# Kernel tuning notes

Hardware: AMD Instinct MI355X
Metric: run time of the kernel (lower is better)

The kernel has to match this reference:

```python
import jax, jax.numpy as jnp
import numpy as np

# model constants (from source: PRE/COMM/OUT sizes; chosen: G, D, E, T, NF)
G, D, E, T = 128, 64, 8, 4096          # group feats, per-elevator feats, n elevators, timesteps
PRE, CI, CH, OUT, NF = 256, 128, 128, 128, 64
ROUNDS, DROPOFF = 3, 0.333
IN = G + D                              # elevator_input_size = 192
OIN = 2 * CH + IN                       # out-LSTM input = 448


def _cell(x, h, c, Wih, Whh, b):
    # torch nn.LSTM cell, gate order i,f,g,o; b = b_ih + b_hh
    g = x @ Wih.T + h @ Whh.T + b
    i, f, gg, o = jnp.split(g, 4, axis=-1)
    c2 = jax.nn.sigmoid(f) * c + jax.nn.sigmoid(i) * jnp.tanh(gg)
    h2 = jax.nn.sigmoid(o) * jnp.tanh(c2)
    return h2, c2


def _forward(features, pre_h0, pre_c0, out_h0, out_c0,
             Wih_p0, Whh_p0, b_p0, Wih_p1, Whh_p1, b_p1, Wfc, bfc,
             Wih_c0, Whh_c0, b_c0, Wih_c1, Whh_c1, b_c1,
             Wih_o, Whh_o, b_o, Wtar, btar, Wdir, bdir):
    def step(carry, feat):
        pre_h, pre_c, out_h, out_c = carry
        group = feat[:G]
        ele = feat[G:].reshape(E, D)
        x = jnp.concatenate([jnp.broadcast_to(group, (E, G)), ele], axis=-1)  # [E, IN]
        # preprocess: 2-layer LSTM single step, batched over elevators
        h0, c0 = _cell(x, pre_h[:, 0], pre_c[:, 0], Wih_p0, Whh_p0, b_p0)
        h1, c1 = _cell(h0, pre_h[:, 1], pre_c[:, 1], Wih_p1, Whh_p1, b_p1)
        pre_out = jax.nn.leaky_relu(h1 @ Wfc.T + bfc, 0.05)                   # [E, CI]
        new_pre_h = jnp.stack([h0, h1], axis=1)
        new_pre_c = jnp.stack([c0, c1], axis=1)
        # alpha-decayed communication rounds: sequential scan over elevators
        ch = jnp.zeros((2, CH), jnp.float32)
        cc = jnp.zeros((2, CH), jnp.float32)
        alpha = 1.0
        for _ in range(ROUNDS):
            def comm_step(cs, xin, alpha=alpha):
                ch_, cc_ = cs
                h0n, c0n = _cell(xin, ch_[0], cc_[0], Wih_c0, Whh_c0, b_c0)
                h0b = (1.0 - alpha) * ch_[0] + alpha * h0n
                c0b = (1.0 - alpha) * cc_[0] + alpha * c0n
                h1n, c1n = _cell(h0b, ch_[1], cc_[1], Wih_c1, Whh_c1, b_c1)
                h1b = (1.0 - alpha) * ch_[1] + alpha * h1n
                c1b = (1.0 - alpha) * cc_[1] + alpha * c1n
                return (jnp.stack([h0b, h1b]), jnp.stack([c0b, c1b])), None
            (ch, cc), _ = jax.lax.scan(comm_step, (ch, cc), pre_out)
            alpha *= DROPOFF
        group_dec = cc.reshape(-1)                                            # [2*CH] = comm_c.flatten()
        out_in = jnp.concatenate([jnp.broadcast_to(group_dec, (E, 2 * CH)), x], axis=-1)  # [E, OIN]
        oh, oc = _cell(out_in, out_h, out_c, Wih_o, Whh_o, b_o)
        tar = jax.nn.softmax(oh @ Wtar.T + btar, axis=-1)                     # [E, NF]
        dr = jax.nn.softmax(oh @ Wdir.T + bdir, axis=-1)                      # [E, 3]
        return (new_pre_h, new_pre_c, oh, oc), (tar, dr)

    _, (tar_seq, dir_seq) = jax.lax.scan(step, (pre_h0, pre_c0, out_h0, out_c0), features)
    return tar_seq, dir_seq


def setup_inputs() -> dict:
    key = jax.random.key(0)
    ks = iter(jax.random.split(key, 32))
    p = lambda *s: jax.random.normal(next(ks), s, jnp.float32) * 0.05
    return {
        "features": jax.random.normal(next(ks), (T, G + E * D), jnp.float32),
        "pre_h0": jnp.zeros((E, 2, PRE), jnp.float32),
        "pre_c0": jnp.zeros((E, 2, PRE), jnp.float32),
        "out_h0": jnp.zeros((E, OUT), jnp.float32),
        "out_c0": jnp.zeros((E, OUT), jnp.float32),
        "Wih_p0": p(4 * PRE, IN), "Whh_p0": p(4 * PRE, PRE), "b_p0": p(4 * PRE),
        "Wih_p1": p(4 * PRE, PRE), "Whh_p1": p(4 * PRE, PRE), "b_p1": p(4 * PRE),
        "Wfc": p(CI, PRE), "bfc": p(CI),
        "Wih_c0": p(4 * CH, CI), "Whh_c0": p(4 * CH, CH), "b_c0": p(4 * CH),
        "Wih_c1": p(4 * CH, CH), "Whh_c1": p(4 * CH, CH), "b_c1": p(4 * CH),
        "Wih_o": p(4 * OUT, OIN), "Whh_o": p(4 * OUT, OUT), "b_o": p(4 * OUT),
        "Wtar": p(NF, OUT), "btar": p(NF),
        "Wdir": p(3, OUT), "bdir": p(3),
    }


def reference(features, pre_h0, pre_c0, out_h0, out_c0,
              Wih_p0, Whh_p0, b_p0, Wih_p1, Whh_p1, b_p1, Wfc, bfc,
              Wih_c0, Whh_c0, b_c0, Wih_c1, Whh_c1, b_c1,
              Wih_o, Whh_o, b_o, Wtar, btar, Wdir, bdir):
    return _forward(features, pre_h0, pre_c0, out_h0, out_c0,
                    Wih_p0, Whh_p0, b_p0, Wih_p1, Whh_p1, b_p1, Wfc, bfc,
                    Wih_c0, Whh_c0, b_c0, Wih_c1, Whh_c1, b_c1,
                    Wih_o, Whh_o, b_o, Wtar, btar, Wdir, bdir)
```

## Files before the change

### kernel.cpp

```cpp
#include <hip/hip_runtime.h>
#include <hip/hip_bf16.h>

#define T_   4096
#define E_   8
#define NCON 176

typedef unsigned long long ull;

__device__ __forceinline__ float sigm(float x)  { return 1.0f / (1.0f + __expf(-x)); }
__device__ __forceinline__ float tanh_(float x) { return 1.0f - 2.0f / (__expf(2.0f * x) + 1.0f); }

__device__ __forceinline__ ull aload64(const ull* p) {
  return __hip_atomic_load(p, __ATOMIC_RELAXED, __HIP_MEMORY_SCOPE_AGENT);
}
__device__ __forceinline__ int aload32(const int* p) {
  return __hip_atomic_load(p, __ATOMIC_RELAXED, __HIP_MEMORY_SCOPE_AGENT);
}
__device__ __forceinline__ float aloadf(const float* p) {
  return __hip_atomic_load(p, __ATOMIC_RELAXED, __HIP_MEMORY_SCOPE_AGENT);
}
__device__ __forceinline__ void lbar() {
  asm volatile("s_waitcnt lgkmcnt(0)\n\ts_barrier" ::: "memory");
}

#define FMA_8(ACC, W, VA, VB)                                   \
  ACC[0] = fmaf((W), (VA).x, ACC[0]); ACC[1] = fmaf((W), (VA).y, ACC[1]); \
  ACC[2] = fmaf((W), (VA).z, ACC[2]); ACC[3] = fmaf((W), (VA).w, ACC[3]); \
  ACC[4] = fmaf((W), (VB).x, ACC[4]); ACC[5] = fmaf((W), (VB).y, ACC[5]); \
  ACC[6] = fmaf((W), (VB).z, ACC[6]); ACC[7] = fmaf((W), (VB).w, ACC[7]);

__global__ void initK(const float* __restrict__ Wih_p0, const float* __restrict__ Whh_p0,
                      const float* __restrict__ Wih_p1, const float* __restrict__ Whh_p1,
                      const float* __restrict__ Wih_c0, const float* __restrict__ Whh_c0,
                      const float* __restrict__ Wih_c1, const float* __restrict__ Whh_c1,
                      const float* __restrict__ Wih_o,
                      float* wt_p0, float* wt_p1, float* wt_c0, float* wt_c1,
                      float* wt_o1, float* wt_o2, int* flags) {
  const int NW = 458752 + 524288 + 131072 + 131072 + 131072 + 98304;
  const int NF = 2 * 64 * 32 * 32 + 512 * 32;
  const int NTOT = NW + NF;
  const int gsz = gridDim.x * blockDim.x;
  for (int i = blockIdx.x * blockDim.x + threadIdx.x; i < NTOT; i += gsz) {
    int idx = i;
    if (idx < 458752) { int k = idx >> 10, c = idx & 1023;
      int wg = c >> 5, r5 = c & 31, gate = r5 >> 3, jl = r5 & 7;
      int col = gate * 256 + wg * 8 + jl;
      wt_p0[idx] = (k < 192) ? Wih_p0[col * 192 + k] : Whh_p0[col * 256 + (k - 192)]; continue; }
    idx -= 458752;
    if (idx < 524288) { int k = idx >> 10, c = idx & 1023;
      int wg = c >> 5, r5 = c & 31, gate = r5 >> 3, jl = r5 & 7;
      int col = gate * 256 + wg * 8 + jl;
      wt_p1[idx] = (k < 256) ? Wih_p1[col * 256 + k] : Whh_p1[col * 256 + (k - 256)]; continue; }
    idx -= 524288;
    if (idx < 131072) { int k = idx >> 9, r = idx & 511;
      wt_c0[idx] = (k < 128) ? Wih_c0[r * 128 + k] : Whh_c0[r * 128 + (k - 128)]; continue; }
    idx -= 131072;
    if (idx < 131072) { int k = idx >> 9, r = idx & 511;
      wt_c1[idx] = (k < 128) ? Wih_c1[r * 128 + k] : Whh_c1[r * 128 + (k - 128)]; continue; }
    idx -= 131072;
    if (idx < 131072) { int k = idx >> 9, r = idx & 511;
      wt_o1[idx] = Wih_o[r * 448 + k]; continue; }
    idx -= 131072;
    if (idx < 98304) { int k = idx >> 9, r = idx & 511;
      wt_o2[idx] = Wih_o[r * 448 + 256 + k]; continue; }
    idx -= 98304;
    flags[idx] = 0;
  }
}

__global__ void opre2K(const float* __restrict__ feat, const float* __restrict__ wt_o2,
                       __hip_bfloat16* __restrict__ opre2) {
  __shared__ float xb[192 * 8];
  const int t = blockIdx.x, tid = threadIdx.x;
  const float* ft = feat + (size_t)t * 640;
  for (int idx = tid; idx < 192 * 8; idx += 256) {
    int k = idx >> 3, e = idx & 7;
    xb[idx] = (k < 128) ? ft[k] : ft[128 + e * 64 + (k - 128)];
  }
  __syncthreads();
  const int r = tid;
  float A0[8] = {0,0,0,0,0,0,0,0};
  float A1[8] = {0,0,0,0,0,0,0,0};
  const float4* x4 = (const float4*)xb;
  #pragma unroll 2
  for (int k = 0; k < 192; ++k) {
    float w0 = wt_o2[k * 512 + r];
    float w1 = wt_o2[k * 512 + 256 + r];
    float4 a = x4[k * 2], b = x4[k * 2 + 1];
    FMA_8(A0, w0, a, b);
    FMA_8(A1, w1, a, b);
  }
  #pragma unroll
  for (int e = 0; e < 8; ++e) {
    opre2[((size_t)t * 8 + e) * 512 + r]       = __float2bfloat16(A0[e]);
    opre2[((size_t)t * 8 + e) * 512 + 256 + r] = __float2bfloat16(A1[e]);
  }
}

__device__ __forceinline__ void comm_cell(
// ... 21 lines not shown
    FMA_8(A0, w0, a, b);
    FMA_8(A1, w1, a, b);
  }
  {
    float4* g4 = (float4*)glb;
    g4[r * 2]             = make_float4(A0[0], A0[1], A0[2], A0[3]);
    g4[r * 2 + 1]         = make_float4(A0[4], A0[5], A0[6], A0[7]);
    g4[(256 + r) * 2]     = make_float4(A1[0], A1[1], A1[2], A1[3]);
    g4[(256 + r) * 2 + 1] = make_float4(A1[4], A1[5], A1[6], A1[7]);
  }
  __syncthreads();
  for (int idx = tid; idx < 1024; idx += 256) {
    int jj = idx >> 3, tt = idx & 7;
    float gi = glb[jj * 8 + tt]         + bias[jj];
    float gf = glb[(128 + jj) * 8 + tt] + bias[128 + jj];
    float gg = glb[(256 + jj) * 8 + tt] + bias[256 + jj];
    float go = glb[(384 + jj) * 8 + tt] + bias[384 + jj];
    float cold = cL[idx], hold = hL[idx];
    float c2 = sigm(gf) * cold + sigm(gi) * tanh_(gg);
    float h2 = sigm(go) * tanh_(c2);
    float hb = fmaf(alpha, h2 - hold, hold);
    float cb = fmaf(alpha, c2 - cold, cold);
    hL[idx] = hb; cL[idx] = cb;
    if (hout) hout[idx] = hb;
  }
  __syncthreads();
}

__launch_bounds__(256, 1)
__global__ void megaK(const float* __restrict__ feat,
                      const float* __restrict__ pre_h0, const float* __restrict__ pre_c0,
                      const float* __restrict__ wt_p0, const float* __restrict__ wt_p1,
                      const float* __restrict__ b_p0, const float* __restrict__ b_p1,
                      float* __restrict__ h0ring, float* __restrict__ h1ring,
                      float* __restrict__ h1all,
                      int* __restrict__ flagsA, int* __restrict__ flagsB,
                      const float* __restrict__ Wfc, const float* __restrict__ bfc,
                      const float* __restrict__ wt_c0, const float* __restrict__ wt_c1,
                      const float* __restrict__ b_c0, const float* __restrict__ b_c1,
                      const float* __restrict__ wt_o1, const float* __restrict__ b_o,
                      float* __restrict__ opre1, int* __restrict__ flagC,
                      const __hip_bfloat16* __restrict__ opre2,
                      const float* __restrict__ Whh_o, const float* __restrict__ out_h0,
                      const float* __restrict__ out_c0, float* __restrict__ oh_g) {
  __shared__ float lds[38912];
  const int wg = blockIdx.x, tid = threadIdx.x;

  if (wg < 32) {
    float* wl   = lds;
    float* xbuf = lds + 14336;
    float* hsf  = lds + 15872;
    float* gl   = lds + 17920;
    const int r5 = tid & 31, kq = tid >> 5;
    for (int idx = tid; idx < 14336; idx += 256)
      wl[idx] = wt_p0[(size_t)(idx >> 5) * 1024 + wg * 32 + (idx & 31)];
    float creg = 0.f, bi = 0.f, bff = 0.f, bg = 0.f, bo = 0.f;
    if (tid < 64) {
      const int jl = tid >> 3, e = tid & 7, j = wg * 8 + jl;
      creg = pre_c0[(e * 2 + 0) * 256 + j];
      bi = b_p0[j]; bff = b_p0[256 + j]; bg = b_p0[512 + j]; bo = b_p0[768 + j];
    }
    for (int idx = tid; idx < 2048; idx += 256) {
      int k = idx >> 3, e = idx & 7;
      hsf[idx] = pre_h0[(e * 2 + 0) * 256 + k];
    }
    for (int idx = tid; idx < 1536; idx += 256) {
      int k = idx >> 3, e = idx & 7;
      xbuf[idx] = (k < 128) ? feat[k] : feat[128 + e * 64 + (k - 128)];
    }
    __syncthreads();
    float Ax[8] = {0,0,0,0,0,0,0,0};
    {
      const float4* x4 = (const float4*)xbuf;
      #pragma unroll
      for (int k = kq * 24; k < kq * 24 + 24; ++k) {
        float w = wl[k * 32 + r5];
        float4 a = x4[k * 2], b = x4[k * 2 + 1];
        FMA_8(Ax, w, a, b);
      }
    }
    for (int t = 0; t < T_; ++t) {
      float px[6];
      if (t + 1 < T_) {
        const float* ft1 = feat + (size_t)(t + 1) * 640;
        #pragma unroll
        for (int i = 0; i < 6; ++i) {
          int idx = tid + i * 256; int k = idx >> 3, e = idx & 7;
          px[i] = (k < 128) ? ft1[k] : ft1[128 + e * 64 + (k - 128)];
        }
      }
      float A[8];
      #pragma unroll
      for (int i = 0; i < 8; ++i) A[i] = Ax[i];
      {
        const float4* h4 = (const float4*)hsf;
        #pragma unroll
        for (int k2 = 0; k2 < 32; ++k2) {
          const int k = kq * 32 + k2;
          float w = wl[(192 + k) * 32 + r5];
          float4 a = h4[k * 2], b = h4[k * 2 + 1];
          FMA_8(A, w, a, b);
        }
      }
      {
        float4* g4 = (float4*)gl;
        g4[(kq * 32 + r5) * 2]     = make_float4(A[0], A[1], A[2], A[3]);
        g4[(kq * 32 + r5) * 2 + 1] = make_float4(A[4], A[5], A[6], A[7]);
      }
      if (tid >= 224 && t >= 8) {
        const int* fp = flagsB + ((size_t)((t - 8) & 63) * 32 + (tid - 224)) * 32;
        while (aload32(fp) < t - 7) __builtin_amdgcn_s_sleep(1);
      }
      lbar();
      if (tid < 64) {
        float s0 = 0.f, s1 = 0.f, s2 = 0.f, s3 = 0.f;
        #pragma unroll
        for (int q = 0; q < 8; ++q) {
          s0 += gl[q * 256 + tid];       s1 += gl[q * 256 + 64 + tid];
          s2 += gl[q * 256 + 128 + tid]; s3 += gl[q * 256 + 192 + tid];
        }
        float c2 = sigm(s1 + bff) * creg + sigm(s0 + bi) * tanh_(s2 + bg);
        float h2 = sigm(s3 + bo) * tanh_(c2);
        creg = c2;
        __hip_atomic_store(&h0ring[(size_t)(t & 7) * 2048 + wg * 64 + tid], h2,
                           __ATOMIC_RELAXED, __HIP_MEMORY_SCOPE_AGENT);
        asm volatile("s_waitcnt vmcnt(0)" ::: "memory");
        if (tid == 0)
          __hip_atomic_store(&flagsA[((size_t)(t & 63) * 32 + wg) * 32], t + 1,
                             __ATOMIC_RELAXED, __HIP_MEMORY_SCOPE_AGENT);
      }
      if (t + 1 >= T_) break;
      #pragma unroll
      for (int i = 0; i < 6; ++i) xbuf[tid + i * 256] = px[i];
      if (tid >= 64 && tid < 96) {
        const int* fp = flagsA + ((size_t)(t & 63) * 32 + (tid - 64)) * 32;
        while (aload32(fp) < t + 1) __builtin_amdgcn_s_sleep(1);
      }
      lbar();
      ull v[4];
      {
        const ull* s8 = (const ull*)(h0ring + (size_t)(t & 7) * 2048);
        #pragma unroll
        for (int i = 0; i < 4; ++i) v[i] = aload64(s8 + tid * 4 + i);
      }
      #pragma unroll
      for (int i = 0; i < 8; ++i) Ax[i] = 0.f;
      {
        const float4* x4 = (const float4*)xbuf;
        #pragma unroll
        for (int k = kq * 24; k < kq * 24 + 24; ++k) {
          float w = wl[k * 32 + r5];
          float4 a = x4[k * 2], b = x4[k * 2 + 1];
          FMA_8(Ax, w, a, b);
        }
      }
      {
        ull* d8 = (ull*)hsf;
        #pragma unroll
        for (int i = 0; i < 4; ++i) d8[tid * 4 + i] = v[i];
      }
      lbar();
    }
  } else if (wg < 64) {
    const int wgl = wg - 32;
    float* wl  = lds;
    float* xh0 = lds + 16384;
    float* hsf = lds + 18432;
    float* gl  = lds + 20480;
    const int r5 = tid & 31, kq = tid >> 5;
    for (int idx = tid; idx < 16384; idx += 256)
      wl[idx] = wt_p1[(size_t)(idx >> 5) * 1024 + wgl * 32 + (idx & 31)];
    float creg = 0.f, bi = 0.f, bff = 0.f, bg = 0.f, bo = 0.f;
    if (tid < 64) {
      const int jl = tid >> 3, e = tid & 7, j = wgl * 8 + jl;
      creg = pre_c0[(e * 2 + 1) * 256 + j];
      bi = b_p1[j]; bff = b_p1[256 + j]; bg = b_p1[512 + j]; bo = b_p1[768 + j];
    }
    for (int idx = tid; idx < 2048; idx += 256) {
      int k = idx >> 3, e = idx & 7;
      hsf[idx] = pre_h0[(e * 2 + 1) * 256 + k];
    }
    __syncthreads();
    if (tid >= 64 && tid < 128) {
      const int lane = tid - 64;
      const int slot = lane >> 5, b = lane & 31;
      const int* fp = flagsA + ((size_t)slot * 32 + b) * 32;
      while (aload32(fp) < slot + 1) __builtin_amdgcn_s_sleep(1);
    }
    __syncthreads();
    ull v0[4];
    {
      const ull* s8 = (const ull*)h0ring;
      #pragma unroll
      for (int i = 0; i < 4; ++i) v0[i] = aload64(s8 + tid * 4 + i);
    }
    {
      ull* d8 = (ull*)xh0;
      #pragma unroll
      for (int i = 0; i < 4; ++i) d8[tid * 4 + i] = v0[i];
    }
    lbar();
    float Ax[8] = {0,0,0,0,0,0,0,0};
    {
      const float4* x4 = (const float4*)xh0;
      #pragma unroll
      for (int k = kq * 32; k < kq * 32 + 32; ++k) {
        float w = wl[k * 32 + r5];
        float4 a = x4[k * 2], b = x4[k * 2 + 1];
        FMA_8(Ax, w, a, b);
      }
    }
    {
      const ull* s8 = (const ull*)(h0ring + 2048);
      #pragma unroll
      for (int i = 0; i < 4; ++i) v0[i] = aload64(s8 + tid * 4 + i);
    }
    for (int t = 0; t < T_; ++t) {
      float A[8];
      #pragma unroll
      for (int i = 0; i < 8; ++i) A[i] = Ax[i];
      {
        const float4* h4 = (const float4*)hsf;
        #pragma unroll
        for (int k2 = 0; k2 < 32; ++k2) {
          const int k = kq * 32 + k2;
          float w = wl[(256 + k) * 32 + r5];
          float4 a = h4[k * 2], b = h4[k * 2 + 1];
          FMA_8(A, w, a, b);
        }
      }
      {
        float4* g4 = (float4*)gl;
        g4[(kq * 32 + r5) * 2]     = make_float4(A[0], A[1], A[2], A[3]);
        g4[(kq * 32 + r5) * 2 + 1] = make_float4(A[4], A[5], A[6], A[7]);
      }
      lbar();
      if (tid < 64) {
        float s0 = 0.f, s1 = 0.f, s2 = 0.f, s3 = 0.f;
        #pragma unroll
        for (int q = 0; q < 8; ++q) {
          s0 += gl[q * 256 + tid];       s1 += gl[q * 256 + 64 + tid];
          s2 += gl[q * 256 + 128 + tid]; s3 += gl[q * 256 + 192 + tid];
        }
        float c2 = sigm(s1 + bff) * creg + sigm(s0 + bi) * tanh_(s2 + bg);
        float h2 = sigm(s3 + bo) * tanh_(c2);
        creg = c2;
        __hip_atomic_store(&h1ring[(size_t)(t & 7) * 2048 + wgl * 64 + tid], h2,
                           __ATOMIC_RELAXED, __HIP_MEMORY_SCOPE_AGENT);
        __hip_atomic_store(&h1all[(size_t)t * 2048 + wgl * 64 + tid], h2,
                           __ATOMIC_RELAXED, __HIP_MEMORY_SCOPE_AGENT);
        asm volatile("s_waitcnt vmcnt(0)" ::: "memory");
        if (tid == 0)
          __hip_atomic_store(&flagsB[((size_t)(t & 63) * 32 + wgl) * 32], t + 1,
                             __ATOMIC_RELAXED, __HIP_MEMORY_SCOPE_AGENT);
      }
      if (t + 1 >= T_) break;
      if (tid >= 64 && tid < 128) {
        const int lane = tid - 64;
        if (lane < 32) {
          const int* fp = flagsB + ((size_t)(t & 63) * 32 + lane) * 32;
          while (aload32(fp) < t + 1) __builtin_amdgcn_s_sleep(1);
        } else if (t + 2 < T_) {
          const int* fp = flagsA + ((size_t)((t + 2) & 63) * 32 + (lane - 32)) * 32;
          while (aload32(fp) < t + 3) __builtin_amdgcn_s_sleep(1);
        }
      }
      lbar();
      ull v1[4];
      {
        const ull* s8 = (const ull*)(h1ring + (size_t)(t & 7) * 2048);
        #pragma unroll
        for (int i = 0; i < 4; ++i) v1[i] = aload64(s8 + tid * 4 + i);
      }
      {
        ull* d8 = (ull*)xh0;
        #pragma unroll
        for (int i = 0; i < 4; ++i) d8[tid * 4 + i] = v0[i];
      }
      lbar();
      if (t + 2 < T_) {
        const ull* s8 = (const ull*)(h0ring + (size_t)((t + 2) & 7) * 2048);
        #pragma unroll
        for (int i = 0; i < 4; ++i) v0[i] = aload64(s8 + tid * 4 + i);
      }
      #pragma unroll
      for (int i = 0; i < 8; ++i) Ax[i] = 0.f;
      {
        const float4* x4 = (const float4*)xh0;
        #pragma unroll
        for (int k = kq * 32; k < kq * 32 + 32; ++k) {
          float w = wl[k * 32 + r5];
          float4 a = x4[k * 2], b = x4[k * 2 + 1];
          FMA_8(Ax, w, a, b);
        }
      }
      {
        ull* d8 = (ull*)hsf;
        #pragma unroll
        for (int i = 0; i < 4; ++i) d8[tid * 4 + i] = v1[i];
      }
      lbar();
    }
  } else if (wg < 72) {
    const int e = wg - 64;
    float* wlds = lds;
    float* ohl  = lds + 32768;
    float* gl   = lds + 32896;
    for (int idx = tid; idx < 32768; idx += 256) {
      int k = idx >> 8, rr = idx & 255;
      wlds[idx] = Whh_o[(256 + rr) * 128 + k];
    }
    float w[128];
    #pragma unroll
    for (int k = 0; k < 128; ++k) w[k] = Whh_o[tid * 128 + k];
    if (tid < 128) ohl[tid] = out_h0[e * 128 + tid];
    float creg = (tid < 128) ? out_c0[e * 128 + tid] : 0.f;
    __syncthreads();
    if (tid == 0) { while (aload32(&flagC[0]) == 0) __builtin_amdgcn_s_sleep(4); }
    __syncthreads();
    const int r0 = tid, r1 = tid + 256;
    float pa = aloadf(&opre1[r0]), pb = aloadf(&opre1[r1]);
    float qa = __bfloat162float(opre2[(size_t)e * 512 + r0]);
    float qb = __bfloat162float(opre2[(size_t)e * 512 + r1]);
    float na = aloadf(&opre1[512 + r0]), nb = aloadf(&opre1[512 + r1]);
    float ma = __bfloat162float(opre2[(size_t)(8 + e) * 512 + r0]);
    float mb = __bfloat162float(opre2[(size_t)(8 + e) * 512 + r1]);
    for (int t = 0; t < T_; ++t) {
      float a0 = pa + qa, a1 = pb + qb;
      pa = na; pb = nb; qa = ma; qb = mb;
      if ((t & 7) == 6 && t + 2 < T_) {
        if (tid == 0) { while (aload32(&flagC[((t + 2) >> 3) * 32]) == 0) __builtin_amdgcn_s_sleep(4); }
        __syncthreads();
      }
      if (t + 2 < T_) {
        na = aloadf(&opre1[(size_t)(t + 2) * 512 + r0]);
        nb = aloadf(&opre1[(size_t)(t + 2) * 512 + r1]);
        ma = __bfloat162float(opre2[((size_t)(t + 2) * 8 + e) * 512 + r0]);
        mb = __bfloat162float(opre2[((size_t)(t + 2) * 8 + e) * 512 + r1]);
      }
      const float4* o4 = (const float4*)ohl;
      #pragma unroll
      for (int kk = 0; kk < 32; ++kk) {
        float4 x = o4[kk];
        a0 = fmaf(w[kk * 4 + 0], x.x, a0); a0 = fmaf(w[kk * 4 + 1], x.y, a0);
        a0 = fmaf(w[kk * 4 + 2], x.z, a0); a0 = fmaf(w[kk * 4 + 3], x.w, a0);
        a1 = fmaf(wlds[(kk * 4 + 0) * 256 + tid], x.x, a1);
        a1 = fmaf(wlds[(kk * 4 + 1) * 256 + tid], x.y, a1);
        a1 = fmaf(wlds[(kk * 4 + 2) * 256 + tid], x.z, a1);
        a1 = fmaf(wlds[(kk * 4 + 3) * 256 + tid], x.w, a1);
      }
      gl[r0] = a0; gl[r1] = a1;
      __syncthreads();
      if (tid < 128) {
        float gi = gl[tid], gf = gl[128 + tid], gg = gl[256 + tid], go = gl[384 + tid];
        float c2 = sigm(gf) * creg + sigm(gi) * tanh_(gg);
        float h2 = sigm(go) * tanh_(c2);
        creg = c2;
        ohl[tid] = h2;
        oh_g[(size_t)t * 1024 + e * 128 + tid] = h2;
      }
      __syncthreads();
    }
  } else {
    const int cb = wg - 72;
    float* h1c    = lds;
    float* polAll = lds + 16384;
    float* ch0 = lds + 24576; float* cc0 = lds + 25600;
    float* ch1 = lds + 26624; float* cc1 = lds + 27648;
    float* h0b = lds + 28672;
    float* glb = lds + 29696;
    for (int chunk = cb; chunk < 512; chunk += NCON) {
      const int t0 = chunk * 8;
      if (tid < 32) {
        const int* fp = flagsB + ((size_t)((t0 + 7) & 63) * 32 + tid) * 32;
        while (aload32(fp) < t0 + 8) __builtin_amdgcn_s_sleep(4);
      }
      __syncthreads();
      {
        const ull* src = (const ull*)(h1all + (size_t)t0 * 2048);
        ull* dst = (ull*)h1c;
        for (int i = tid; i < 8192; i += 256) dst[i] = aload64(src + i);
      }
      __syncthreads();
      {
        const int c = tid >> 1, half = tid & 1;
        const float bv = bfc[c];
        const float* wrow = Wfc + c * 256;
        for (int tt = 0; tt < 8; ++tt) {
          float a0 = bv, a1 = bv, a2 = bv, a3 = bv;
          const float4* h4 = (const float4*)(h1c + tt * 2048);
          #pragma unroll 4
          for (int k = 0; k < 256; ++k) {
            float wv = wrow[k];
            float4 x = h4[k * 2 + half];
            a0 = fmaf(wv, x.x, a0); a1 = fmaf(wv, x.y, a1);
            a2 = fmaf(wv, x.z, a2); a3 = fmaf(wv, x.w, a3);
          }
          float vv[4] = {a0, a1, a2, a3};
          #pragma unroll
          for (int i = 0; i < 4; ++i) {
            float v = vv[i];
            v = (v > 0.f) ? v : 0.05f * v;
            polAll[(half * 4 + i) * 1024 + c * 8 + tt] = v;
          }
        }
      }
      for (int idx = tid; idx < 1024; idx += 256) { ch0[idx]=0.f; cc0[idx]=0.f; ch1[idx]=0.f; cc1[idx]=0.f; }
      __syncthreads();
// ... 98 lines not shown
  const float* Wih_p1 = (const float*)d_in[8];
  const float* Whh_p1 = (const float*)d_in[9];
  const float* b_p1   = (const float*)d_in[10];
  const float* Wfc    = (const float*)d_in[11];
  const float* bfc    = (const float*)d_in[12];
  const float* Wih_c0 = (const float*)d_in[13];
  const float* Whh_c0 = (const float*)d_in[14];
  const float* b_c0   = (const float*)d_in[15];
  const float* Wih_c1 = (const float*)d_in[16];
  const float* Whh_c1 = (const float*)d_in[17];
  const float* b_c1   = (const float*)d_in[18];
  const float* Wih_o  = (const float*)d_in[19];
  const float* Whh_o  = (const float*)d_in[20];
  const float* b_o    = (const float*)d_in[21];
  const float* Wtar   = (const float*)d_in[22];
  const float* btar   = (const float*)d_in[23];
  const float* Wdir   = (const float*)d_in[24];
  const float* bdir   = (const float*)d_in[25];
  float* outp = (float*)d_out;

  float* ws = (float*)d_ws;
  size_t off = 0;
  float* opre1    = ws + off; off += (size_t)T_ * 512;
  float* oh_g     = ws + off; off += (size_t)T_ * E_ * 128;
  float* wt_p0    = ws + off; off += (size_t)448 * 1024;
  float* wt_p1    = ws + off; off += (size_t)512 * 1024;
  float* wt_c0    = ws + off; off += (size_t)256 * 512;
  float* wt_c1    = ws + off; off += (size_t)256 * 512;
  float* wt_o1    = ws + off; off += (size_t)256 * 512;
  float* wt_o2    = ws + off; off += (size_t)192 * 512;
  __hip_bfloat16* opre2 = (__hip_bfloat16*)(ws + off);
  off += (size_t)T_ * E_ * 512 / 2;
  float* h1all  = ws + off; off += (size_t)T_ * 2048;
  float* h0ring = ws + off; off += (size_t)8 * 2048;
  float* h1ring = ws + off; off += (size_t)8 * 2048;
  int* flags    = (int*)(ws + off);
  int* flagsA   = flags;
  int* flagsB   = flags + (size_t)64 * 32 * 32;
  int* flagC    = flags + (size_t)2 * 64 * 32 * 32;

  initK<<<dim3(1024), dim3(256), 0, stream>>>(
      Wih_p0, Whh_p0, Wih_p1, Whh_p1, Wih_c0, Whh_c0, Wih_c1, Whh_c1, Wih_o,
      wt_p0, wt_p1, wt_c0, wt_c1, wt_o1, wt_o2, flags);
  opre2K<<<dim3(T_), dim3(256), 0, stream>>>(feat, wt_o2, opre2);
  megaK<<<dim3(32 + 32 + 8 + NCON), dim3(256), 0, stream>>>(
      feat, pre_h0, pre_c0, wt_p0, wt_p1, b_p0, b_p1,
      h0ring, h1ring, h1all, flagsA, flagsB,
      Wfc, bfc, wt_c0, wt_c1, b_c0, b_c1, wt_o1, b_o, opre1, flagC,
      opre2, Whh_o, out_h0, out_c0, oh_g);
  phaseD<<<dim3(T_), dim3(64), 0, stream>>>(oh_g, Wtar, btar, Wdir, bdir, outp);
}
```

Baseline: 16.66 ms.

## Merge preprocess LSTM layers into one workgroup set with tagged-value ring sync

The two preprocess LSTM layers, previously run by separate 32-workgroup groups, now run in the same 32 workgroups. Layer 1 lags layer 0 by one timestep, so each step needs a single cross-workgroup exchange instead of two chained ones. Consumers poll 3-bit generation tags packed into the low mantissa bits of the ring values instead of waiting on separate flags, and the freed workgroups go to more comm consumers with a longer sleep. This cuts per-step synchronisation latency on the serial critical path. In exchange it perturbs the low bits of every exchanged hidden value and adds more LDS and FMA work per workgroup.

Result: slower. 25.25 ms (+51.6%).

```diff
diff --git a/kernel.cpp b/kernel.cpp
--- a/kernel.cpp
+++ b/kernel.cpp
@@ -3,7 +3,7 @@
 
 #define T_   4096
 #define E_   8
-#define NCON 176
+#define NCON 208
 
 typedef unsigned long long ull;
 
@@ -19,6 +19,10 @@
 __device__ __forceinline__ float aloadf(const float* p) {
   return __hip_atomic_load(p, __ATOMIC_RELAXED, __HIP_MEMORY_SCOPE_AGENT);
 }
+__device__ __forceinline__ float tagf(float h, unsigned g) {
+  return __uint_as_float((__float_as_uint(h) & ~7u) | g);
+}
+__device__ __forceinline__ float u2f(unsigned u) { return __uint_as_float(u); }
 __device__ __forceinline__ void lbar() {
   asm volatile("s_waitcnt lgkmcnt(0)\n\ts_barrier" ::: "memory");
 }
@@ -35,10 +39,10 @@
                       const float* __restrict__ Wih_c1, const float* __restrict__ Whh_c1,
                       const float* __restrict__ Wih_o,
                       float* wt_p0, float* wt_p1, float* wt_c0, float* wt_c1,
-                      float* wt_o1, float* wt_o2, int* flags) {
+                      float* wt_o1, float* wt_o2, int* zbase) {
   const int NW = 458752 + 524288 + 131072 + 131072 + 131072 + 98304;
-  const int NF = 2 * 64 * 32 * 32 + 512 * 32;
-  const int NTOT = NW + NF;
+  const int NZ = 32768 + 1024 + 65536 + 16384;
+  const int NTOT = NW + NZ;
   const int gsz = gridDim.x * blockDim.x;
   for (int i = blockIdx.x * blockDim.x + threadIdx.x; i < NTOT; i += gsz) {
     int idx = i;
@@ -64,7 +68,7 @@
     if (idx < 98304) { int k = idx >> 9, r = idx & 511;
       wt_o2[idx] = Wih_o[r * 448 + 256 + k]; continue; }
     idx -= 98304;
-    flags[idx] = 0;
+    zbase[idx] = 0;
   }
 }
 
@@ -152,9 +156,8 @@
                       const float* __restrict__ pre_h0, const float* __restrict__ pre_c0,
                       const float* __restrict__ wt_p0, const float* __restrict__ wt_p1,
                       const float* __restrict__ b_p0, const float* __restrict__ b_p1,
-                      float* __restrict__ h0ring, float* __restrict__ h1ring,
-                      float* __restrict__ h1all,
-                      int* __restrict__ flagsA, int* __restrict__ flagsB,
+                      float* __restrict__ ringM, int* __restrict__ flagsM,
+                      float* __restrict__ h1all, int* __restrict__ flagsBC,
                       const float* __restrict__ Wfc, const float* __restrict__ bfc,
                       const float* __restrict__ wt_c0, const float* __restrict__ wt_c1,
                       const float* __restrict__ b_c0, const float* __restrict__ b_c1,
@@ -163,38 +166,49 @@
                       const __hip_bfloat16* __restrict__ opre2,
                       const float* __restrict__ Whh_o, const float* __restrict__ out_h0,
                       const float* __restrict__ out_c0, float* __restrict__ oh_g) {
-  __shared__ float lds[38912];
+  __shared__ float lds[40448];
   const int wg = blockIdx.x, tid = threadIdx.x;
 
   if (wg < 32) {
-    float* wl   = lds;
-    float* xbuf = lds + 14336;
-    float* hsf  = lds + 15872;
-    float* gl   = lds + 17920;
+    float* wl0  = lds;
+    float* wl1  = lds + 14336;
+    float* xbuf = lds + 30720;
+    float* h0sf = lds + 32256;
+    float* h1sf = lds + 34304;
+    float* gl0  = lds + 36352;
+    float* gl1  = lds + 38400;
     const int r5 = tid & 31, kq = tid >> 5;
     for (int idx = tid; idx < 14336; idx += 256)
-      wl[idx] = wt_p0[(size_t)(idx >> 5) * 1024 + wg * 32 + (idx & 31)];
-    float creg = 0.f, bi = 0.f, bff = 0.f, bg = 0.f, bo = 0.f;
+      wl0[idx] = wt_p0[(size_t)(idx >> 5) * 1024 + wg * 32 + (idx & 31)];
+    for (int idx = tid; idx < 16384; idx += 256)
+      wl1[idx] = wt_p1[(size_t)(idx >> 5) * 1024 + wg * 32 + (idx & 31)];
+    float creg = 0.f, bi = 0.f, bff = 0.f, bgg = 0.f, bo = 0.f;
     if (tid < 64) {
       const int jl = tid >> 3, e = tid & 7, j = wg * 8 + jl;
       creg = pre_c0[(e * 2 + 0) * 256 + j];
-      bi = b_p0[j]; bff = b_p0[256 + j]; bg = b_p0[512 + j]; bo = b_p0[768 + j];
+      bi = b_p0[j]; bff = b_p0[256 + j]; bgg = b_p0[512 + j]; bo = b_p0[768 + j];
+    } else if (tid < 128) {
+      const int l = tid - 64, jl = l >> 3, e = l & 7, j = wg * 8 + jl;
+      creg = pre_c0[(e * 2 + 1) * 256 + j];
+      bi = b_p1[j]; bff = b_p1[256 + j]; bgg = b_p1[512 + j]; bo = b_p1[768 + j];
     }
     for (int idx = tid; idx < 2048; idx += 256) {
-      int k = idx >> 3, e = idx & 7;
-      hsf[idx] = pre_h0[(e * 2 + 0) * 256 + k];
+      const int k = idx >> 3, e = idx & 7;
+      h0sf[idx] = pre_h0[(e * 2 + 0) * 256 + k];
+      h1sf[idx] = pre_h0[(e * 2 + 1) * 256 + k];
     }
     for (int idx = tid; idx < 1536; idx += 256) {
-      int k = idx >> 3, e = idx & 7;
+      const int k = idx >> 3, e = idx & 7;
       xbuf[idx] = (k < 128) ? feat[k] : feat[128 + e * 64 + (k - 128)];
     }
     __syncthreads();
+    const bool own = ((tid >> 3) == wg);
     float Ax[8] = {0,0,0,0,0,0,0,0};
     {
       const float4* x4 = (const float4*)xbuf;
       #pragma unroll
       for (int k = kq * 24; k < kq * 24 + 24; ++k) {
-        float w = wl[k * 32 + r5];
+        float w = wl0[k * 32 + r5];
         float4 a = x4[k * 2], b = x4[k * 2 + 1];
         FMA_8(Ax, w, a, b);
       }
@@ -209,220 +223,191 @@
           px[i] = (k < 128) ? ft1[k] : ft1[128 + e * 64 + (k - 128)];
         }
       }
-      float A[8];
+      float A0[8], A1[8];
       #pragma unroll
-      for (int i = 0; i < 8; ++i) A[i] = Ax[i];
-      {
-        const float4* h4 = (const float4*)hsf;
+      for (int i = 0; i < 8; ++i) { A0[i] = Ax[i]; A1[i] = 0.f; }
+      {
+        const float4* h4 = (const float4*)h0sf;
         #pragma unroll
         for (int k2 = 0; k2 < 32; ++k2) {
           const int k = kq * 32 + k2;
-          float w = wl[(192 + k) * 32 + r5];
+          float w0 = wl0[(192 + k) * 32 + r5];
+          float w1 = wl1[k * 32 + r5];
           float4 a = h4[k * 2], b = h4[k * 2 + 1];
-          FMA_8(A, w, a, b);
-        }
-      }
-      {
-        float4* g4 = (float4*)gl;
-        g4[(kq * 32 + r5) * 2]     = make_float4(A[0], A[1], A[2], A[3]);
-        g4[(kq * 32 + r5) * 2 + 1] = make_float4(A[4], A[5], A[6], A[7]);
-      }
-      if (tid >= 224 && t >= 8) {
-        const int* fp = flagsB + ((size_t)((t - 8) & 63) * 32 + (tid - 224)) * 32;
-        while (aload32(fp) < t - 7) __builtin_amdgcn_s_sleep(1);
+          FMA_8(A0, w0, a, b);
+          FMA_8(A1, w1, a, b);
+        }
+      }
+      {
+        const float4* h4 = (const float4*)h1sf;
+        #pragma unroll
+        for (int k2 = 0; k2 < 32; ++k2) {
+          const int k = kq * 32 + k2;
+          float w = wl1[(256 + k) * 32 + r5];
+          float4 a = h4[k * 2], b = h4[k * 2 + 1];
+          FMA_8(A1, w, a, b);
+        }
+      }
+      {
+        float4* g4 = (float4*)gl0;
+        g4[(kq * 32 + r5) * 2]     = make_float4(A0[0], A0[1], A0[2], A0[3]);
+        g4[(kq * 32 + r5) * 2 + 1] = make_float4(A0[4], A0[5], A0[6], A0[7]);
+        float4* g5 = (float4*)gl1;
+        g5[(kq * 32 + r5) * 2]     = make_float4(A1[0], A1[1], A1[2], A1[3]);
+        g5[(kq * 32 + r5) * 2 + 1] = make_float4(A1[4], A1[5], A1[6], A1[7]);
       }
       lbar();
+      const unsigned g = ((unsigned)(t >> 3) % 7u) + 1u;
+      float* ringS = ringM + (size_t)(t & 7) * 4096;
       if (tid < 64) {
         float s0 = 0.f, s1 = 0.f, s2 = 0.f, s3 = 0.f;
         #pragma unroll
         for (int q = 0; q < 8; ++q) {
-          s0 += gl[q * 256 + tid];       s1 += gl[q * 256 + 64 + tid];
-          s2 += gl[q * 256 + 128 + tid]; s3 += gl[q * 256 + 192 + tid];
-        }
-        float c2 = sigm(s1 + bff) * creg + sigm(s0 + bi) * tanh_(s2 + bg);
+          s0 += gl0[q * 256 + tid];       s1 += gl0[q * 256 + 64 + tid];
+          s2 += gl0[q * 256 + 128 + tid]; s3 += gl0[q * 256 + 192 + tid];
+        }
+        float c2 = sigm(s1 + bff) * creg + sigm(s0 + bi) * tanh_(s2 + bgg);
         float h2 = sigm(s3 + bo) * tanh_(c2);
         creg = c2;
-        __hip_atomic_store(&h0ring[(size_t)(t & 7) * 2048 + wg * 64 + tid], h2,
+        __hip_atomic_store(&ringS[wg * 128 + tid], tagf(h2, g),
+                           __ATOMIC_RELAXED, __HIP_MEMORY_SCOPE_AGENT);
+        h0sf[wg * 64 + tid] = h2;
+      } else if (tid < 128) {
+        const int l = tid - 64;
+        float h2;
+        if (t > 0) {
+          float s0 = 0.f, s1 = 0.f, s2 = 0.f, s3 = 0.f;
+          #pragma unroll
+          for (int q = 0; q < 8; ++q) {
+            s0 += gl1[q * 256 + l];       s1 += gl1[q * 256 + 64 + l];
+            s2 += gl1[q * 256 + 128 + l]; s3 += gl1[q * 256 + 192 + l];
+          }
+          float c2 = sigm(s1 + bff) * creg + sigm(s0 + bi) * tanh_(s2 + bgg);
+          h2 = sigm(s3 + bo) * tanh_(c2);
+          creg = c2;
+          __hip_atomic_store(&h1all[(size_t)(t - 1) * 2048 + wg * 64 + l], h2,
+                             __ATOMIC_RELAXED, __HIP_MEMORY_SCOPE_AGENT);
+          h1sf[wg * 64 + l] = h2;
+        } else {
+          h2 = h1sf[wg * 64 + l];
+        }
+        __hip_atomic_store(&ringS[wg * 128 + 64 + l], tagf(h2, g),
+                           __ATOMIC_RELAXED, __HIP_MEMORY_SCOPE_AGENT);
+        if (l == 0)
+          __hip_atomic_store(&flagsM[wg * 32], t + 1,
+                             __ATOMIC_RELAXED, __HIP_MEMORY_SCOPE_AGENT);
+        if (t > 0 && ((t - 1) & 7) == 7) {
+          asm volatile("s_waitcnt vmcnt(0)" ::: "memory");
+          if (l == 0)
+            __hip_atomic_store(&flagsBC[((size_t)((t - 1) & 63) * 32 + wg) * 32], t,
+                               __ATOMIC_RELAXED, __HIP_MEMORY_SCOPE_AGENT);
+        }
+      } else if (tid < 160) {
+        const int p = tid - 128;
+        if (p != wg) {
+          const int* fp = flagsM + p * 32;
+          while (aload32(fp) < t + 1) __builtin_amdgcn_s_sleep(1);
+        }
+      }
+      lbar();
+      ull v[8];
+      const ull* rp = (const ull*)ringS + tid * 8;
+      if (!own) {
+        #pragma unroll
+        for (int i = 0; i < 8; ++i) v[i] = aload64(rp + i);
+      }
+      if (t + 1 < T_) {
+        #pragma unroll
+        for (int i = 0; i < 6; ++i) xbuf[tid + i * 256] = px[i];
+      }
+      lbar();
+      #pragma unroll
+      for (int i = 0; i < 8; ++i) Ax[i] = 0.f;
+      {
+        const float4* x4 = (const float4*)xbuf;
+        #pragma unroll
+        for (int k = kq * 24; k < kq * 24 + 24; ++k) {
+          float w = wl0[k * 32 + r5];
+          float4 a = x4[k * 2], b = x4[k * 2 + 1];
+          FMA_8(Ax, w, a, b);
+        }
+      }
+      if (!own) {
+        while (true) {
+          bool ok = true;
+          #pragma unroll
+          for (int i = 0; i < 8; ++i) {
+            unsigned lo = (unsigned)v[i], hi = (unsigned)(v[i] >> 32);
+            ok &= ((lo & 7u) == g) & ((hi & 7u) == g);
+          }
+          if (ok) break;
+          __builtin_amdgcn_s_sleep(1);
+          #pragma unroll
+          for (int i = 0; i < 8; ++i) v[i] = aload64(rp + i);
+        }
+        const int p8 = tid >> 3, q8 = tid & 7;
+        float* dst = (q8 < 4) ? (h0sf + p8 * 64 + q8 * 16)
+                              : (h1sf + p8 * 64 + (q8 - 4) * 16);
+        float4* d4 = (float4*)dst;
+        d4[0] = make_float4(u2f((unsigned)v[0]), u2f((unsigned)(v[0] >> 32)),
+                            u2f((unsigned)v[1]), u2f((unsigned)(v[1] >> 32)));
+        d4[1] = make_float4(u2f((unsigned)v[2]), u2f((unsigned)(v[2] >> 32)),
+                            u2f((unsigned)v[3]), u2f((unsigned)(v[3] >> 32)));
+        d4[2] = make_float4(u2f((unsigned)v[4]), u2f((unsigned)(v[4] >> 32)),
+                            u2f((unsigned)v[5]), u2f((unsigned)(v[5] >> 32)));
+        d4[3] = make_float4(u2f((unsigned)v[6]), u2f((unsigned)(v[6] >> 32)),
+                            u2f((unsigned)v[7]), u2f((unsigned)(v[7] >> 32)));
+      }
+      lbar();
+    }
+    {
+      float A1[8] = {0,0,0,0,0,0,0,0};
+      {
+        const float4* h4 = (const float4*)h0sf;
+        #pragma unroll
+        for (int k2 = 0; k2 < 32; ++k2) {
+          const int k = kq * 32 + k2;
+          float w = wl1[k * 32 + r5];
+          float4 a = h4[k * 2], b = h4[k * 2 + 1];
+          FMA_8(A1, w, a, b);
+        }
+      }
+      {
+        const float4* h4 = (const float4*)h1sf;
+        #pragma unroll
+        for (int k2 = 0; k2 < 32; ++k2) {
+          const int k = kq * 32 + k2;
+          float w = wl1[(256 + k) * 32 + r5];
+          float4 a = h4[k * 2], b = h4[k * 2 + 1];
+          FMA_8(A1, w, a, b);
+        }
+      }
+      {
+        float4* g5 = (float4*)gl1;
+        g5[(kq * 32 + r5) * 2]     = make_float4(A1[0], A1[1], A1[2], A1[3]);
+        g5[(kq * 32 + r5) * 2 + 1] = make_float4(A1[4], A1[5], A1[6], A1[7]);
+      }
+      lbar();
+      if (tid >= 64 && tid < 128) {
+        const int l = tid - 64;
+        float s0 = 0.f, s1 = 0.f, s2 = 0.f, s3 = 0.f;
+        #pragma unroll
+        for (int q = 0; q < 8; ++q) {
+          s0 += gl1[q * 256 + l];       s1 += gl1[q * 256 + 64 + l];
+          s2 += gl1[q * 256 + 128 + l]; s3 += gl1[q * 256 + 192 + l];
+        }
+        float c2 = sigm(s1 + bff) * creg + sigm(s0 + bi) * tanh_(s2 + bgg);
+        float h2 = sigm(s3 + bo) * tanh_(c2);
+        __hip_atomic_store(&h1all[(size_t)(T_ - 1) * 2048 + wg * 64 + l], h2,
                            __ATOMIC_RELAXED, __HIP_MEMORY_SCOPE_AGENT);
         asm volatile("s_waitcnt vmcnt(0)" ::: "memory");
-        if (tid == 0)
-          __hip_atomic_store(&flagsA[((size_t)(t & 63) * 32 + wg) * 32], t + 1,
+        if (l == 0)
+          __hip_atomic_store(&flagsBC[((size_t)((T_ - 1) & 63) * 32 + wg) * 32], T_,
                              __ATOMIC_RELAXED, __HIP_MEMORY_SCOPE_AGENT);
       }
-      if (t + 1 >= T_) break;
-      #pragma unroll
-      for (int i = 0; i < 6; ++i) xbuf[tid + i * 256] = px[i];
-      if (tid >= 64 && tid < 96) {
-        const int* fp = flagsA + ((size_t)(t & 63) * 32 + (tid - 64)) * 32;
-        while (aload32(fp) < t + 1) __builtin_amdgcn_s_sleep(1);
-      }
-      lbar();
-      ull v[4];
-      {
-        const ull* s8 = (const ull*)(h0ring + (size_t)(t & 7) * 2048);
-        #pragma unroll
-        for (int i = 0; i < 4; ++i) v[i] = aload64(s8 + tid * 4 + i);
-      }
-      #pragma unroll
-      for (int i = 0; i < 8; ++i) Ax[i] = 0.f;
-      {
-        const float4* x4 = (const float4*)xbuf;
-        #pragma unroll
-        for (int k = kq * 24; k < kq * 24 + 24; ++k) {
-          float w = wl[k * 32 + r5];
-          float4 a = x4[k * 2], b = x4[k * 2 + 1];
-          FMA_8(Ax, w, a, b);
-        }
-      }
-      {
-        ull* d8 = (ull*)hsf;
-        #pragma unroll
-        for (int i = 0; i < 4; ++i) d8[tid * 4 + i] = v[i];
-      }
-      lbar();
-    }
-  } else if (wg < 64) {
-    const int wgl = wg - 32;
-    float* wl  = lds;
-    float* xh0 = lds + 16384;
-    float* hsf = lds + 18432;
-    float* gl  = lds + 20480;
-    const int r5 = tid & 31, kq = tid >> 5;
-    for (int idx = tid; idx < 16384; idx += 256)
-      wl[idx] = wt_p1[(size_t)(idx >> 5) * 1024 + wgl * 32 + (idx & 31)];
-    float creg = 0.f, bi = 0.f, bff = 0.f, bg = 0.f, bo = 0.f;
-    if (tid < 64) {
-      const int jl = tid >> 3, e = tid & 7, j = wgl * 8 + jl;
-      creg = pre_c0[(e * 2 + 1) * 256 + j];
-      bi = b_p1[j]; bff = b_p1[256 + j]; bg = b_p1[512 + j]; bo = b_p1[768 + j];
-    }
-    for (int idx = tid; idx < 2048; idx += 256) {
-      int k = idx >> 3, e = idx & 7;
-      hsf[idx] = pre_h0[(e * 2 + 1) * 256 + k];
-    }
-    __syncthreads();
-    if (tid >= 64 && tid < 128) {
-      const int lane = tid - 64;
-      const int slot = lane >> 5, b = lane & 31;
-      const int* fp = flagsA + ((size_t)slot * 32 + b) * 32;
-      while (aload32(fp) < slot + 1) __builtin_amdgcn_s_sleep(1);
-    }
-    __syncthreads();
-    ull v0[4];
-    {
-      const ull* s8 = (const ull*)h0ring;
-      #pragma unroll
-      for (int i = 0; i < 4; ++i) v0[i] = aload64(s8 + tid * 4 + i);
-    }
-    {
-      ull* d8 = (ull*)xh0;
-      #pragma unroll
-      for (int i = 0; i < 4; ++i) d8[tid * 4 + i] = v0[i];
-    }
-    lbar();
-    float Ax[8] = {0,0,0,0,0,0,0,0};
-    {
-      const float4* x4 = (const float4*)xh0;
-      #pragma unroll
-      for (int k = kq * 32; k < kq * 32 + 32; ++k) {
-        float w = wl[k * 32 + r5];
-        float4 a = x4[k * 2], b = x4[k * 2 + 1];
-        FMA_8(Ax, w, a, b);
-      }
-    }
-    {
-      const ull* s8 = (const ull*)(h0ring + 2048);
-      #pragma unroll
-      for (int i = 0; i < 4; ++i) v0[i] = aload64(s8 + tid * 4 + i);
-    }
-    for (int t = 0; t < T_; ++t) {
-      float A[8];
-      #pragma unroll
-      for (int i = 0; i < 8; ++i) A[i] = Ax[i];
-      {
-        const float4* h4 = (const float4*)hsf;
-        #pragma unroll
-        for (int k2 = 0; k2 < 32; ++k2) {
-          const int k = kq * 32 + k2;
-          float w = wl[(256 + k) * 32 + r5];
-          float4 a = h4[k * 2], b = h4[k * 2 + 1];
-          FMA_8(A, w, a, b);
-        }
-      }
-      {
-        float4* g4 = (float4*)gl;
-        g4[(kq * 32 + r5) * 2]     = make_float4(A[0], A[1], A[2], A[3]);
-        g4[(kq * 32 + r5) * 2 + 1] = make_float4(A[4], A[5], A[6], A[7]);
-      }
-      lbar();
-      if (tid < 64) {
-        float s0 = 0.f, s1 = 0.f, s2 = 0.f, s3 = 0.f;
-        #pragma unroll
-        for (int q = 0; q < 8; ++q) {
-          s0 += gl[q * 256 + tid];       s1 += gl[q * 256 + 64 + tid];
-          s2 += gl[q * 256 + 128 + tid]; s3 += gl[q * 256 + 192 + tid];
-        }
-        float c2 = sigm(s1 + bff) * creg + sigm(s0 + bi) * tanh_(s2 + bg);
-        float h2 = sigm(s3 + bo) * tanh_(c2);
-        creg = c2;
-        __hip_atomic_store(&h1ring[(size_t)(t & 7) * 2048 + wgl * 64 + tid], h2,
-                           __ATOMIC_RELAXED, __HIP_MEMORY_SCOPE_AGENT);
-        __hip_atomic_store(&h1all[(size_t)t * 2048 + wgl * 64 + tid], h2,
-                           __ATOMIC_RELAXED, __HIP_MEMORY_SCOPE_AGENT);
-        asm volatile("s_waitcnt vmcnt(0)" ::: "memory");
-        if (tid == 0)
-          __hip_atomic_store(&flagsB[((size_t)(t & 63) * 32 + wgl) * 32], t + 1,
-                             __ATOMIC_RELAXED, __HIP_MEMORY_SCOPE_AGENT);
-      }
-      if (t + 1 >= T_) break;
-      if (tid >= 64 && tid < 128) {
-        const int lane = tid - 64;
-        if (lane < 32) {
-          const int* fp = flagsB + ((size_t)(t & 63) * 32 + lane) * 32;
-          while (aload32(fp) < t + 1) __builtin_amdgcn_s_sleep(1);
-        } else if (t + 2 < T_) {
-          const int* fp = flagsA + ((size_t)((t + 2) & 63) * 32 + (lane - 32)) * 32;
-          while (aload32(fp) < t + 3) __builtin_amdgcn_s_sleep(1);
-        }
-      }
-      lbar();
-      ull v1[4];
-      {
-        const ull* s8 = (const ull*)(h1ring + (size_t)(t & 7) * 2048);
-        #pragma unroll
-        for (int i = 0; i < 4; ++i) v1[i] = aload64(s8 + tid * 4 + i);
-      }
-      {
-        ull* d8 = (ull*)xh0;
-        #pragma unroll
-        for (int i = 0; i < 4; ++i) d8[tid * 4 + i] = v0[i];
-      }
-      lbar();
-      if (t + 2 < T_) {
-        const ull* s8 = (const ull*)(h0ring + (size_t)((t + 2) & 7) * 2048);
-        #pragma unroll
-        for (int i = 0; i < 4; ++i) v0[i] = aload64(s8 + tid * 4 + i);
-      }
-      #pragma unroll
-      for (int i = 0; i < 8; ++i) Ax[i] = 0.f;
-      {
-        const float4* x4 = (const float4*)xh0;
-        #pragma unroll
-        for (int k = kq * 32; k < kq * 32 + 32; ++k) {
-          float w = wl[k * 32 + r5];
-          float4 a = x4[k * 2], b = x4[k * 2 + 1];
-          FMA_8(Ax, w, a, b);
-        }
-      }
-      {
-        ull* d8 = (ull*)hsf;
-        #pragma unroll
-        for (int i = 0; i < 4; ++i) d8[tid * 4 + i] = v1[i];
-      }
-      lbar();
-    }
-  } else if (wg < 72) {
-    const int e = wg - 64;
+    }
+  } else if (wg < 40) {
+    const int e = wg - 32;
     float* wlds = lds;
     float* ohl  = lds + 32768;
     float* gl   = lds + 32896;
@@ -482,7 +467,7 @@
       __syncthreads();
     }
   } else {
-    const int cb = wg - 72;
+    const int cb = wg - 40;
     float* h1c    = lds;
     float* polAll = lds + 16384;
     float* ch0 = lds + 24576; float* cc0 = lds + 25600;
@@ -492,8 +477,8 @@
     for (int chunk = cb; chunk < 512; chunk += NCON) {
       const int t0 = chunk * 8;
       if (tid < 32) {
-        const int* fp = flagsB + ((size_t)((t0 + 7) & 63) * 32 + tid) * 32;
-        while (aload32(fp) < t0 + 8) __builtin_amdgcn_s_sleep(4);
+        const int* fp = flagsBC + ((size_t)((t0 + 7) & 63) * 32 + tid) * 32;
+        while (aload32(fp) < t0 + 8) __builtin_amdgcn_s_sleep(64);
       }
       __syncthreads();
       {
@@ -658,20 +643,20 @@
   __hip_bfloat16* opre2 = (__hip_bfloat16*)(ws + off);
   off += (size_t)T_ * E_ * 512 / 2;
   float* h1all  = ws + off; off += (size_t)T_ * 2048;
-  float* h0ring = ws + off; off += (size_t)8 * 2048;
-  float* h1ring = ws + off; off += (size_t)8 * 2048;
+  float* ringM  = ws + off; off += (size_t)8 * 4096;
   int* flags    = (int*)(ws + off);
-  int* flagsA   = flags;
-  int* flagsB   = flags + (size_t)64 * 32 * 32;
-  int* flagC    = flags + (size_t)2 * 64 * 32 * 32;
+  int* flagsM   = flags;
+  int* flagsBC  = flags + (size_t)32 * 32;
+  int* flagC    = flags + (size_t)32 * 32 + (size_t)64 * 32 * 32;
+  int* zbase    = (int*)ringM;
 
   initK<<<dim3(1024), dim3(256), 0, stream>>>(
       Wih_p0, Whh_p0, Wih_p1, Whh_p1, Wih_c0, Whh_c0, Wih_c1, Whh_c1, Wih_o,
-      wt_p0, wt_p1, wt_c0, wt_c1, wt_o1, wt_o2, flags);
+      wt_p0, wt_p1, wt_c0, wt_c1, wt_o1, wt_o2, zbase);
   opre2K<<<dim3(T_), dim3(256), 0, stream>>>(feat, wt_o2, opre2);
-  megaK<<<dim3(32 + 32 + 8 + NCON), dim3(256), 0, stream>>>(
+  megaK<<<dim3(32 + 8 + NCON), dim3(256), 0, stream>>>(
       feat, pre_h0, pre_c0, wt_p0, wt_p1, b_p0, b_p1,
-      h0ring, h1ring, h1all, flagsA, flagsB,
+      ringM, flagsM, h1all, flagsBC,
       Wfc, bfc, wt_c0, wt_c1, b_c0, b_c1, wt_o1, b_o, opre1, flagC,
       opre2, Whh_o, out_h0, out_c0, oh_g);
   phaseD<<<dim3(T_), dim3(64), 0, stream>>>(oh_g, Wtar, btar, Wdir, bdir, outp);
```

## Decouple layer-1 step flags from chunk flags and defer h1all publication off critical path

Applied to the files above, without the earlier changes.

Splits the layer-1 per-step flag into a fast step flag used by the recurrent pipeline and a separate chunk flag published every 8 steps for consumer blocks. The global h1all store is moved out of the critical store-then-flag sequence and done after the barrier by a spare warp, with the h0 ring enlarged to 32 slots so layer-0 can run further ahead of consumers. Backpressure polling becomes coarser with longer sleeps. The aim is to shorten the serial recurrence latency per timestep, at the cost of more complex flag bookkeeping and looser lookahead bounds.

Result: slower. 18.01 ms (+8.1%).

```diff
diff --git a/kernel.cpp b/kernel.cpp
--- a/kernel.cpp
+++ b/kernel.cpp
@@ -35,10 +35,10 @@
                       const float* __restrict__ Wih_c1, const float* __restrict__ Whh_c1,
                       const float* __restrict__ Wih_o,
                       float* wt_p0, float* wt_p1, float* wt_c0, float* wt_c1,
-                      float* wt_o1, float* wt_o2, int* flags) {
+                      float* wt_o1, float* wt_o2, int* zbase) {
   const int NW = 458752 + 524288 + 131072 + 131072 + 131072 + 98304;
-  const int NF = 2 * 64 * 32 * 32 + 512 * 32;
-  const int NTOT = NW + NF;
+  const int NZ = 65536 + 16384 + 65536 + 65536 + 65536 + 16384;
+  const int NTOT = NW + NZ;
   const int gsz = gridDim.x * blockDim.x;
   for (int i = blockIdx.x * blockDim.x + threadIdx.x; i < NTOT; i += gsz) {
     int idx = i;
@@ -64,7 +64,7 @@
     if (idx < 98304) { int k = idx >> 9, r = idx & 511;
       wt_o2[idx] = Wih_o[r * 448 + 256 + k]; continue; }
     idx -= 98304;
-    flags[idx] = 0;
+    zbase[idx] = 0;
   }
 }
 
@@ -154,7 +154,8 @@
                       const float* __restrict__ b_p0, const float* __restrict__ b_p1,
                       float* __restrict__ h0ring, float* __restrict__ h1ring,
                       float* __restrict__ h1all,
-                      int* __restrict__ flagsA, int* __restrict__ flagsB,
+                      int* __restrict__ flagsA, int* __restrict__ flagB1,
+                      int* __restrict__ flagsBC,
                       const float* __restrict__ Wfc, const float* __restrict__ bfc,
                       const float* __restrict__ wt_c0, const float* __restrict__ wt_c1,
                       const float* __restrict__ b_c0, const float* __restrict__ b_c1,
@@ -227,9 +228,10 @@
         g4[(kq * 32 + r5) * 2]     = make_float4(A[0], A[1], A[2], A[3]);
         g4[(kq * 32 + r5) * 2 + 1] = make_float4(A[4], A[5], A[6], A[7]);
       }
-      if (tid >= 224 && t >= 8) {
-        const int* fp = flagsB + ((size_t)((t - 8) & 63) * 32 + (tid - 224)) * 32;
-        while (aload32(fp) < t - 7) __builtin_amdgcn_s_sleep(1);
+      if (t >= 24 && tid >= 224) {
+        const int t2 = (t - 24) | 7;
+        const int* fp = flagsBC + ((size_t)(t2 & 63) * 32 + (tid - 224)) * 32;
+        while (aload32(fp) < t2 + 1) __builtin_amdgcn_s_sleep(16);
       }
       lbar();
       if (tid < 64) {
@@ -242,7 +244,7 @@
         float c2 = sigm(s1 + bff) * creg + sigm(s0 + bi) * tanh_(s2 + bg);
         float h2 = sigm(s3 + bo) * tanh_(c2);
         creg = c2;
-        __hip_atomic_store(&h0ring[(size_t)(t & 7) * 2048 + wg * 64 + tid], h2,
+        __hip_atomic_store(&h0ring[(size_t)(t & 31) * 2048 + wg * 64 + tid], h2,
                            __ATOMIC_RELAXED, __HIP_MEMORY_SCOPE_AGENT);
         asm volatile("s_waitcnt vmcnt(0)" ::: "memory");
         if (tid == 0)
@@ -259,7 +261,7 @@
       lbar();
       ull v[4];
       {
-        const ull* s8 = (const ull*)(h0ring + (size_t)(t & 7) * 2048);
+        const ull* s8 = (const ull*)(h0ring + (size_t)(t & 31) * 2048);
         #pragma unroll
         for (int i = 0; i < 4; ++i) v[i] = aload64(s8 + tid * 4 + i);
       }
@@ -367,18 +369,17 @@
         creg = c2;
         __hip_atomic_store(&h1ring[(size_t)(t & 7) * 2048 + wgl * 64 + tid], h2,
                            __ATOMIC_RELAXED, __HIP_MEMORY_SCOPE_AGENT);
-        __hip_atomic_store(&h1all[(size_t)t * 2048 + wgl * 64 + tid], h2,
-                           __ATOMIC_RELAXED, __HIP_MEMORY_SCOPE_AGENT);
+        hsf[wgl * 64 + tid] = h2;
         asm volatile("s_waitcnt vmcnt(0)" ::: "memory");
         if (tid == 0)
-          __hip_atomic_store(&flagsB[((size_t)(t & 63) * 32 + wgl) * 32], t + 1,
+          __hip_atomic_store(&flagB1[((size_t)(t & 63) * 32 + wgl) * 32], t + 1,
                              __ATOMIC_RELAXED, __HIP_MEMORY_SCOPE_AGENT);
       }
       if (t + 1 >= T_) break;
       if (tid >= 64 && tid < 128) {
         const int lane = tid - 64;
         if (lane < 32) {
-          const int* fp = flagsB + ((size_t)(t & 63) * 32 + lane) * 32;
+          const int* fp = flagB1 + ((size_t)(t & 63) * 32 + lane) * 32;
           while (aload32(fp) < t + 1) __builtin_amdgcn_s_sleep(1);
         } else if (t + 2 < T_) {
           const int* fp = flagsA + ((size_t)((t + 2) & 63) * 32 + (lane - 32)) * 32;
@@ -386,6 +387,18 @@
         }
       }
       lbar();
+      if (tid >= 192) {
+        const int l = tid - 192;
+        float h2o = hsf[wgl * 64 + l];
+        __hip_atomic_store(&h1all[(size_t)t * 2048 + wgl * 64 + l], h2o,
+                           __ATOMIC_RELAXED, __HIP_MEMORY_SCOPE_AGENT);
+        if ((t & 7) == 7) {
+          asm volatile("s_waitcnt vmcnt(0)" ::: "memory");
+          if (l == 0)
+            __hip_atomic_store(&flagsBC[((size_t)(t & 63) * 32 + wgl) * 32], t + 1,
+                               __ATOMIC_RELAXED, __HIP_MEMORY_SCOPE_AGENT);
+        }
+      }
       ull v1[4];
       {
         const ull* s8 = (const ull*)(h1ring + (size_t)(t & 7) * 2048);
@@ -399,7 +412,7 @@
       }
       lbar();
       if (t + 2 < T_) {
-        const ull* s8 = (const ull*)(h0ring + (size_t)((t + 2) & 7) * 2048);
+        const ull* s8 = (const ull*)(h0ring + (size_t)((t + 2) & 31) * 2048);
         #pragma unroll
         for (int i = 0; i < 4; ++i) v0[i] = aload64(s8 + tid * 4 + i);
       }
@@ -420,6 +433,17 @@
         for (int i = 0; i < 4; ++i) d8[tid * 4 + i] = v1[i];
       }
       lbar();
+    }
+    lbar();
+    if (tid >= 192) {
+      const int l = tid - 192;
+      float h2o = hsf[wgl * 64 + l];
+      __hip_atomic_store(&h1all[(size_t)(T_ - 1) * 2048 + wgl * 64 + l], h2o,
+                         __ATOMIC_RELAXED, __HIP_MEMORY_SCOPE_AGENT);
+      asm volatile("s_waitcnt vmcnt(0)" ::: "memory");
+      if (l == 0)
+        __hip_atomic_store(&flagsBC[((size_t)((T_ - 1) & 63) * 32 + wgl) * 32], T_,
+                           __ATOMIC_RELAXED, __HIP_MEMORY_SCOPE_AGENT);
     }
   } else if (wg < 72) {
     const int e = wg - 64;
@@ -492,8 +516,8 @@
     for (int chunk = cb; chunk < 512; chunk += NCON) {
       const int t0 = chunk * 8;
       if (tid < 32) {
-        const int* fp = flagsB + ((size_t)((t0 + 7) & 63) * 32 + tid) * 32;
-        while (aload32(fp) < t0 + 8) __builtin_amdgcn_s_sleep(4);
+        const int* fp = flagsBC + ((size_t)((t0 + 7) & 63) * 32 + tid) * 32;
+        while (aload32(fp) < t0 + 8) __builtin_amdgcn_s_sleep(64);
       }
       __syncthreads();
       {
@@ -658,20 +682,22 @@
   __hip_bfloat16* opre2 = (__hip_bfloat16*)(ws + off);
   off += (size_t)T_ * E_ * 512 / 2;
   float* h1all  = ws + off; off += (size_t)T_ * 2048;
-  float* h0ring = ws + off; off += (size_t)8 * 2048;
+  float* h0ring = ws + off; off += (size_t)32 * 2048;
   float* h1ring = ws + off; off += (size_t)8 * 2048;
   int* flags    = (int*)(ws + off);
   int* flagsA   = flags;
-  int* flagsB   = flags + (size_t)64 * 32 * 32;
-  int* flagC    = flags + (size_t)2 * 64 * 32 * 32;
+  int* flagB1   = flags + (size_t)64 * 32 * 32;
+  int* flagsBC  = flags + (size_t)2 * 64 * 32 * 32;
+  int* flagC    = flags + (size_t)3 * 64 * 32 * 32;
+  int* zbase    = (int*)h0ring;
 
   initK<<<dim3(1024), dim3(256), 0, stream>>>(
       Wih_p0, Whh_p0, Wih_p1, Whh_p1, Wih_c0, Whh_c0, Wih_c1, Whh_c1, Wih_o,
-      wt_p0, wt_p1, wt_c0, wt_c1, wt_o1, wt_o2, flags);
+      wt_p0, wt_p1, wt_c0, wt_c1, wt_o1, wt_o2, zbase);
   opre2K<<<dim3(T_), dim3(256), 0, stream>>>(feat, wt_o2, opre2);
   megaK<<<dim3(32 + 32 + 8 + NCON), dim3(256), 0, stream>>>(
       feat, pre_h0, pre_c0, wt_p0, wt_p1, b_p0, b_p1,
-      h0ring, h1ring, h1all, flagsA, flagsB,
+      h0ring, h1ring, h1all, flagsA, flagB1, flagsBC,
       Wfc, bfc, wt_c0, wt_c1, b_c0, b_c1, wt_o1, b_o, opre1, flagC,
       opre2, Whh_o, out_h0, out_c0, oh_g);
   phaseD<<<dim3(T_), dim3(64), 0, stream>>>(oh_g, Wtar, btar, Wdir, bdir, outp);
```
